# Kernel optimization log

Hardware: AMD Instinct MI355X
Metric: run time of the kernel (lower is better)

The kernel has to match this reference:

```python
import jax, jax.numpy as jnp
import numpy as np

M1 = 12; M2 = 12; WIDTH = 32; NR = 16; GROUPS = 2; EPS = 1e-5
AND_M = 5; AND_LAM = 1e-4; AND_MAXIT = 16; AND_BETA = 1.0
B = 4; H = 192; W = 192


def group_norm(x, w, b, groups=GROUPS, eps=EPS):
    bb, c, hh, ww = x.shape
    xg = x.reshape(bb, groups, c // groups, hh, ww)
    mu = xg.mean(axis=(2, 3, 4), keepdims=True)
    var = xg.var(axis=(2, 3, 4), keepdims=True)
    xn = ((xg - mu) / jnp.sqrt(var + eps)).reshape(bb, c, hh, ww)
    return xn * w[None, :, None, None] + b[None, :, None, None]


def spectral_conv(z, w1, w2):
    bb, c, hh, ww = z.shape
    zf = jnp.fft.rfft2(z, axes=(-2, -1))  # (B,C,H,W//2+1) complex64
    top = jnp.einsum('bixy,ioxy->boxy', zf[:, :, :M1, :M2], w1)
    bot = jnp.einsum('bixy,ioxy->boxy', zf[:, :, hh - M1:, :M2], w2)
    out = jnp.zeros(zf.shape, zf.dtype)
    out = out.at[:, :, :M1, :M2].set(top).at[:, :, hh - M1:, :M2].set(bot)
    return jnp.fft.irfft2(out, s=(hh, ww), axes=(-2, -1))


def f_block(z, xin, p):
    (conv_w, gnw, gnb, q_w, q_b, w1r, w1i, w2r, w2i,
     w0w, w0b, n1w, n1b, n2w, n2b) = p
    # ConvInjection: conv3x3 -> GroupNorm -> channel Linear -> sigmoid
    xi = jax.lax.conv_general_dilated(xin, conv_w, (1, 1), 'SAME',
                                      dimension_numbers=('NCHW', 'OIHW', 'NCHW'))
    xi = group_norm(xi, gnw, gnb)
    xi = jax.nn.sigmoid(jnp.einsum('bnhw,dn->bdhw', xi, q_w) + q_b[None, :, None, None])
    # FourierLayer: spectral conv + 1x1 conv, gelu
    y1 = spectral_conv(z, jax.lax.complex(w1r, w1i), jax.lax.complex(w2r, w2i))
    y2 = jnp.einsum('bchw,oc->bohw', z, w0w) + w0b[None, :, None, None]
    y = jax.nn.gelu(y1 + y2, approximate=False)
    return group_norm(jax.nn.relu(z + group_norm(xi + y, n1w, n1b)), n2w, n2b)


def anderson(f, x0, m=AND_M, lam=AND_LAM, max_iter=AND_MAXIT, beta=AND_BETA):
    """Anderson acceleration; fixed iteration count (tol early-exit omitted)."""
    shp = x0.shape
    bsz = shp[0]
    fv = lambda v: f(v.reshape(shp)).reshape(bsz, -1)
    x0v = x0.reshape(bsz, -1)
    d = x0v.shape[1]
    f0 = fv(x0v)
    f1 = fv(f0)
    X = jnp.zeros((bsz, m, d), x0.dtype).at[:, 0].set(x0v).at[:, 1].set(f0)
    Fm = jnp.zeros((bsz, m, d), x0.dtype).at[:, 0].set(f0).at[:, 1].set(f1)
    last = 1
    for k in range(2, max_iter):
        n = min(k, m)
        G = Fm[:, :n] - X[:, :n]
        Hk = jnp.zeros((bsz, n + 1, n + 1), x0.dtype)
        Hk = Hk.at[:, 0, 1:].set(1.0).at[:, 1:, 0].set(1.0)
        Hk = Hk.at[:, 1:, 1:].set(jnp.einsum('bnd,bmd->bnm', G, G)
                                  + lam * jnp.eye(n, dtype=x0.dtype)[None])
        yk = jnp.zeros((bsz, n + 1, 1), x0.dtype).at[:, 0, 0].set(1.0)
        alpha = jnp.linalg.solve(Hk, yk)[:, 1:, 0]  # (B, n)
        xnew = (beta * jnp.einsum('bn,bnd->bd', alpha, Fm[:, :n])
                + (1.0 - beta) * jnp.einsum('bn,bnd->bd', alpha, X[:, :n]))
        X = X.at[:, k % m].set(xnew)
        Fm = Fm.at[:, k % m].set(fv(xnew))
        last = k % m
    return X[:, last].reshape(shp)


def setup_inputs():
    key = jax.random.key(0)
    ks = jax.random.split(key, 16)
    scale = 1.0 / (WIDTH * WIDTH)
    u = lambda k, shp, s: jax.random.uniform(k, shp, jnp.float32, -s, s)
    return {
        'x': jax.random.normal(ks[0], (B, 1, H, W), jnp.float32),
        'fc0_w': u(ks[1], (WIDTH, 1), 1.0),
        'fc0_b': u(ks[2], (WIDTH,), 1.0),
        'conv_w': 0.01 * jax.random.normal(ks[3], (NR, WIDTH, 3, 3), jnp.float32),
        'inj_gn_w': jnp.ones((NR,), jnp.float32),
        'inj_gn_b': jnp.zeros((NR,), jnp.float32),
        'q_w': 0.01 * jax.random.normal(ks[4], (WIDTH, NR), jnp.float32),
        'q_b': u(ks[5], (WIDTH,), 0.25),
        'sw1r': scale * jax.random.uniform(ks[6], (WIDTH, WIDTH, M1, M2), jnp.float32),
        'sw1i': scale * jax.random.uniform(ks[7], (WIDTH, WIDTH, M1, M2), jnp.float32),
        'sw2r': scale * jax.random.uniform(ks[8], (WIDTH, WIDTH, M1, M2), jnp.float32),
        'sw2i': scale * jax.random.uniform(ks[9], (WIDTH, WIDTH, M1, M2), jnp.float32),
        'w0_w': u(ks[10], (WIDTH, WIDTH), 1.0 / np.sqrt(WIDTH)),
        'w0_b': u(ks[11], (WIDTH,), 1.0 / np.sqrt(WIDTH)),
        'n1_w': jnp.ones((WIDTH,), jnp.float32),
        'n1_b': jnp.zeros((WIDTH,), jnp.float32),
        'n2_w': jnp.ones((WIDTH,), jnp.float32),
        'n2_b': jnp.zeros((WIDTH,), jnp.float32),
        'bn_w': jnp.ones((WIDTH,), jnp.float32),
        'bn_b': jnp.zeros((WIDTH,), jnp.float32),
        'fc1_w': u(ks[12], (32, WIDTH), 1.0 / np.sqrt(WIDTH)),
        'fc1_b': u(ks[13], (32,), 1.0 / np.sqrt(WIDTH)),
        'fc2_w': u(ks[14], (1, 32), 1.0 / np.sqrt(32.0)),
        'fc2_b': u(ks[15], (1,), 1.0 / np.sqrt(32.0)),
    }


def reference(x, fc0_w, fc0_b, conv_w, inj_gn_w, inj_gn_b, q_w, q_b,
              sw1r, sw1i, sw2r, sw2i, w0_w, w0_b, n1_w, n1_b, n2_w, n2_b,
              bn_w, bn_b, fc1_w, fc1_b, fc2_w, fc2_b):
    xin = jnp.einsum('bchw,oc->bohw', x, fc0_w) + fc0_b[None, :, None, None]
    p = (conv_w, inj_gn_w, inj_gn_b, q_w, q_b, sw1r, sw1i, sw2r, sw2i,
         w0_w, w0_b, n1_w, n1_b, n2_w, n2_b)
    z_star = anderson(lambda z: f_block(z, xin, p), jnp.zeros_like(xin))
    z = f_block(z_star, xin, p)
    # BatchNorm2d (training-mode batch statistics, biased var)
    mu = z.mean(axis=(0, 2, 3), keepdims=True)
    var = z.var(axis=(0, 2, 3), keepdims=True)
    zb = (z - mu) / jnp.sqrt(var + EPS) * bn_w[None, :, None, None] + bn_b[None, :, None, None]
    h1 = jax.nn.gelu(jnp.einsum('bchw,oc->bohw', zb, fc1_w) + fc1_b[None, :, None, None],
                     approximate=False)
    return jnp.einsum('bchw,oc->bohw', h1, fc2_w) + fc2_b[None, :, None, None]
```

## Files before the change

### kernel.cpp

```cpp
#include <hip/hip_runtime.h>
#include <math.h>

#ifndef M_PI
#define M_PI 3.14159265358979323846
#endif

#define BBc 4
#define CCc 32
#define NRk 16
#define HHc 192
#define WWc 192
#define HWc 36864
#define DDi 1179648
#define M1c 12
#define EPSc 1e-5f

static const size_t DDs = (size_t)DDi;

#define SZ_T   ((size_t)4718592)
#define SZ_ZC  ((size_t)589824)
#define SZ_ZF  ((size_t)73728)
#define SZ_WT  ((size_t)589824)
#define SZ_TAB ((size_t)4992)

#define OFF_XC   ((size_t)0)
#define OFF_XI   (OFF_XC + SZ_T)
#define OFF_F    (OFF_XI + SZ_T)
#define OFF_G    (OFF_F + 5 * SZ_T)
#define OFF_ZC   (OFF_G + 5 * SZ_T)
#define OFF_ZF   (OFF_ZC + SZ_ZC)
#define OFF_MO   (OFF_ZF + SZ_ZF)
#define OFF_TM   (OFF_MO + SZ_ZF)
#define OFF_WT   (OFF_TM + SZ_ZC)
#define OFF_TAB  (OFF_WT + SZ_WT)
#define OFF_STAT (OFF_TAB + SZ_TAB)
#define A_XI0  OFF_G

#define NSLICE  32
#define NGSLICE 16
#define ST_EV   1024
#define ST_INJ   (16 * ST_EV)
#define ST_BN    (ST_INJ + 16)
#define ST_GRAM  (ST_BN + 64)
#define ST_ALPHA (ST_GRAM + NGSLICE * 60)
#define ST_TOTAL (ST_ALPHA + 20)

__device__ __forceinline__ float bf2f(unsigned short u) {
    return __uint_as_float(((unsigned int)u) << 16);
}
__device__ __forceinline__ unsigned short f2bf(float f) {
    unsigned int u = __float_as_uint(f);
    unsigned int r = (u + 0x7FFFu + ((u >> 16) & 1u)) >> 16;
    return (unsigned short)r;
}

__global__ void k_zero(float* p, int n) {
    int i = blockIdx.x * blockDim.x + threadIdx.x;
    if (i < n) p[i] = 0.f;
}

__global__ void k_tables(float* tab) {
    int i = blockIdx.x * blockDim.x + threadIdx.x;
    if (i < 13 * 192) {
        int k = i / 192, x = i % 192;
        double th = 2.0 * M_PI * (double)(k * x) / 192.0;
        tab[i] = (float)cos(th);
        tab[13 * 192 + i] = (float)sin(th);
    }
}

__global__ void k_wt(const float* __restrict__ w1r, const float* __restrict__ w1i,
                     const float* __restrict__ w2r, const float* __restrict__ w2i,
                     float* __restrict__ wt) {
    int idx = blockIdx.x * 256 + threadIdx.x;
    if (idx >= 24 * 12 * 1024) return;
    int o = idx & 31;
    int i = (idx >> 5) & 31;
    int ky = (idx >> 10) % 12;
    int j = idx / (12 * 1024);
    const float* wr;
    const float* wi;
    int x;
    if (j < 12) { wr = w1r; wi = w1i; x = j; }
    else        { wr = w2r; wi = w2i; x = j - 12; }
    int src = ((i * 32 + o) * 12 + x) * 12 + ky;
    size_t dst = (((size_t)ky * 24 + j) * 1024 + i * 32 + o) * 2;
    wt[dst] = wr[src];
    wt[dst + 1] = wi[src];
}

__global__ void k_ew(const float* __restrict__ cw, const float* __restrict__ fc0w,
                     const float* __restrict__ fc0b, float* __restrict__ ewb) {
    int i = threadIdx.x;
    if (i >= 144) return;
    int n = i / 9, t = i % 9;
    float ew = 0.f, eb = 0.f;
    for (int c = 0; c < 32; ++c) {
        float k = cw[(size_t)(n * CCc + c) * 9 + t];
        ew += k * fc0w[c];
        eb += k * fc0b[c];
    }
    ewb[i] = ew;
    ewb[144 + i] = eb;
}

__global__ __launch_bounds__(192) void k_conv2(const float* __restrict__ x,
                                               const float* __restrict__ ewb,
                                               float* __restrict__ xi0) {
    int b = blockIdx.x / HHc, h = blockIdx.x % HHc;
    __shared__ float sm[3 * 194];
    __shared__ float ews[144], ebs[144];
    int w = threadIdx.x;
    for (int i = threadIdx.x; i < 3 * 194; i += 192) {
        int r = i / 194, col = (i % 194) - 1;
        int hr = h + r - 1;
        float v = 0.f;
        if (hr >= 0 && hr < HHc && col >= 0 && col < WWc)
            v = x[(size_t)b * HWc + (size_t)hr * WWc + col];
        sm[i] = v;
    }
    if (threadIdx.x < 144) {
        ews[threadIdx.x] = ewb[threadIdx.x];
        ebs[threadIdx.x] = ewb[144 + threadIdx.x];
    }
    __syncthreads();
    float xv[9], mk[9];
#pragma unroll
    for (int r = 0; r < 3; ++r) {
        int hr = h + r - 1;
        bool rok = (hr >= 0 && hr < HHc);
#pragma unroll
        for (int dx = 0; dx < 3; ++dx) {
            int wx = w + dx - 1;
            bool ok = rok && (wx >= 0) && (wx < WWc);
            xv[r * 3 + dx] = sm[r * 194 + (w + dx)];
            mk[r * 3 + dx] = ok ? 1.f : 0.f;
        }
    }
#pragma unroll
    for (int n = 0; n < 16; ++n) {
        float acc = 0.f;
#pragma unroll
        for (int t = 0; t < 9; ++t)
            acc += ews[n * 9 + t] * xv[t] + mk[t] * ebs[n * 9 + t];
        xi0[((size_t)b * NRk + n) * HWc + (size_t)h * WWc + w] = acc;
    }
}

__global__ void k_binstats(const float* __restrict__ src, float* __restrict__ stats,
                           int binsize, int blocksPerBin) {
    int bin = blockIdx.x / blocksPerBin, sub = blockIdx.x % blocksPerBin;
    const float* p = src + (size_t)bin * binsize;
    float s = 0.f, q = 0.f;
    for (int i = sub * blockDim.x + threadIdx.x; i < binsize; i += blocksPerBin * blockDim.x) {
        float v = p[i];
        s += v;
        q += v * v;
    }
    for (int o = 32; o; o >>= 1) { s += __shfl_down(s, o); q += __shfl_down(q, o); }
    __shared__ float rs[4], rq[4];
    int wid = threadIdx.x >> 6, lane = threadIdx.x & 63;
    if (lane == 0) { rs[wid] = s; rq[wid] = q; }
    __syncthreads();
    if (threadIdx.x == 0) {
        int nw = blockDim.x >> 6;
        float ts = 0.f, tq = 0.f;
        for (int i = 0; i < nw; ++i) { ts += rs[i]; tq += rq[i]; }
        atomicAdd(&stats[bin * 2], ts);
        atomicAdd(&stats[bin * 2 + 1], tq);
    }
}

__global__ __launch_bounds__(192) void k_xi(const float* __restrict__ xi0,
                                            const float* __restrict__ stats,
                                            const float* __restrict__ gnw, const float* __restrict__ gnb,
                                            const float* __restrict__ qw, const float* __restrict__ qb,
                                            float* __restrict__ xi) {
    int b = blockIdx.x / HHc, h = blockIdx.x % HHc;
    int w = threadIdx.x;
    const float Ninv = 1.f / (8.f * HWc);
    float tn[16];
#pragma unroll
    for (int n = 0; n < 16; ++n) {
        int g = n >> 3;
        float su = stats[(b * 2 + g) * 2], sq = stats[(b * 2 + g) * 2 + 1];
        float mu = su * Ninv;
        float var = sq * Ninv - mu * mu;
        float inv = rsqrtf(var + EPSc);
        float v = xi0[((size_t)b * NRk + n) * HWc + (size_t)h * WWc + w];
        tn[n] = (v - mu) * inv * gnw[n] + gnb[n];
    }
#pragma unroll
    for (int d = 0; d < 32; ++d) {
        float acc = qb[d];
        const float* row = qw + d * 16;
#pragma unroll
        for (int n = 0; n < 16; ++n) acc += tn[n] * row[n];
        xi[((size_t)b * CCc + d) * HWc + (size_t)h * WWc + w] = 1.f / (1.f + expf(-acc));
    }
}


__global__ __launch_bounds__(192) void k_dftw(const float* __restrict__ z0,
                                              const float* __restrict__ tab,
                                              float* __restrict__ Zc) {
    int bc = blockIdx.x / 24;
    int hg = blockIdx.x % 24;
    int b = bc >> 5, c = bc & 31;
    const float* zp = z0 + (size_t)b * DDs + (size_t)c * HWc + (size_t)hg * 8 * WWc;
    __shared__ float rows[8 * 196];
    __shared__ float tb[24 * 196];
    const float4* zq = (const float4*)zp;
    for (int i4 = threadIdx.x; i4 < 384; i4 += 192) {
        float4 v = zq[i4];
        int r = i4 / 48, col = (i4 % 48) * 4;
        *(float4*)&rows[r * 196 + col] = v;
    }
    for (int i4 = threadIdx.x; i4 < 1152; i4 += 192) {
        int rr = i4 / 48, col = (i4 % 48) * 4;
        const float* src = (rr < 12) ? &tab[rr * 192 + col] : &tab[2496 + (rr - 12) * 192 + col];
        *(float4*)&tb[rr * 196 + col] = *(const float4*)src;
    }
    __syncthreads();
    int t = threadIdx.x;
    int r = t / 24, q = t % 24, ky = q >> 1, isim = q & 1;
    const float* tbp = tb + (isim ? (12 + ky) * 196 : ky * 196);
    const float* rowp = rows + r * 196;
    float a0 = 0.f, a1 = 0.f, a2 = 0.f, a3 = 0.f;
#pragma unroll
    for (int w2 = 0; w2 < WWc; w2 += 4) {
        a0 += rowp[w2] * tbp[w2];
        a1 += rowp[w2 + 1] * tbp[w2 + 1];
        a2 += rowp[w2 + 2] * tbp[w2 + 2];
        a3 += rowp[w2 + 3] * tbp[w2 + 3];
    }
    float acc = (a0 + a1) + (a2 + a3);
    if (isim) acc = -acc;
    int h = hg * 8 + r;
    Zc[(((size_t)ky * 128 + bc) * HHc + h) * 2 + isim] = acc;
}

__global__ __launch_bounds__(192) void k_dftwx(const float* __restrict__ F,
                                               const float* __restrict__ gram,
                                               const float* __restrict__ tab,
                                               float* __restrict__ xc,
                                               float* __restrict__ Zc,
                                               int n) {
    int bc = blockIdx.x / 24;
    int hg = blockIdx.x % 24;
    int b = bc >> 5, c = bc & 31;
    __shared__ float rows[8 * 196];
    __shared__ float tb[24 * 196];
    __shared__ float gs[15];
    __shared__ float alf[5];
    for (int i4 = threadIdx.x; i4 < 1152; i4 += 192) {
        int rr = i4 / 48, col = (i4 % 48) * 4;
        const float* src = (rr < 12) ? &tab[rr * 192 + col] : &tab[2496 + (rr - 12) * 192 + col];
        *(float4*)&tb[rr * 196 + col] = *(const float4*)src;
    }
    if (threadIdx.x < 15) {
        float v = 0.f;
        for (int s2 = 0; s2 < NGSLICE; ++s2) v += gram[s2 * 60 + b * 15 + threadIdx.x];
        gs[threadIdx.x] = v;
    }
    __syncthreads();
    if (threadIdx.x == 0) {
        float H[5][5];
#pragma unroll
        for (int i = 0; i < 5; ++i)
#pragma unroll
            for (int j = 0; j <= i; ++j) {
                float v;
                if (i < n && j < n) v = gs[i * (i + 1) / 2 + j] + ((i == j) ? 1e-4f : 0.f);
                else                v = (i == j) ? 1.f : 0.f;
                H[i][j] = v;
                H[j][i] = v;
            }
        float L[5][5], D[5], w[5], y[5];
#pragma unroll
        for (int j = 0; j < 5; ++j) {
            float d = H[j][j];
#pragma unroll
            for (int k2 = 0; k2 < j; ++k2) d -= L[j][k2] * L[j][k2] * D[k2];
            D[j] = d;
#pragma unroll
            for (int i = j + 1; i < 5; ++i) {
                float v = H[i][j];
#pragma unroll
                for (int k2 = 0; k2 < j; ++k2) v -= L[i][k2] * L[j][k2] * D[k2];
                L[i][j] = v / d;
            }
        }
#pragma unroll
        for (int i = 0; i < 5; ++i) {
            float v = (i < n) ? 1.f : 0.f;
#pragma unroll
            for (int k2 = 0; k2 < i; ++k2) v -= L[i][k2] * w[k2];
            w[i] = v;
        }
#pragma unroll
        for (int i = 4; i >= 0; --i) {
            float v = w[i] / D[i];
#pragma unroll
            for (int k2 = i + 1; k2 < 5; ++k2) v -= L[k2][i] * y[k2];
            y[i] = v;
        }
        float sum = y[0] + y[1] + y[2] + y[3] + y[4];
        float inv = 1.f / sum;
#pragma unroll
        for (int j = 0; j < 5; ++j) alf[j] = (j < n) ? y[j] * inv : 0.f;
    }
    __syncthreads();
    float a0 = alf[0], a1 = alf[1], a2 = alf[2], a3 = alf[3], a4 = alf[4];

    size_t elem = (size_t)b * DDs + (size_t)c * HWc + (size_t)hg * 8 * WWc;
    int off4 = (int)(elem >> 2);
    const int sq4 = 1179648;
    const float4* F4 = (const float4*)F;
    float4* xc4 = (float4*)xc;
    for (int i4 = threadIdx.x; i4 < 384; i4 += 192) {
        float4 f0 = F4[off4 + i4];
        float4 f1 = F4[sq4 + off4 + i4];
        float4 f2 = F4[2 * sq4 + off4 + i4];
        float4 f3 = F4[3 * sq4 + off4 + i4];
        float4 f4v = F4[4 * sq4 + off4 + i4];
        float4 v;
        v.x = a0 * f0.x + a1 * f1.x + a2 * f2.x + a3 * f3.x + a4 * f4v.x;
        v.y = a0 * f0.y + a1 * f1.y + a2 * f2.y + a3 * f3.y + a4 * f4v.y;
        v.z = a0 * f0.z + a1 * f1.z + a2 * f2.z + a3 * f3.z + a4 * f4v.z;
        v.w = a0 * f0.w + a1 * f1.w + a2 * f2.w + a3 * f3.w + a4 * f4v.w;
        xc4[off4 + i4] = v;
        int r = i4 / 48, col = (i4 % 48) * 4;
        *(float4*)&rows[r * 196 + col] = v;
    }
    __syncthreads();
    int t = threadIdx.x;
    int r = t / 24, q = t % 24, ky = q >> 1, isim = q & 1;
    const float* tbp = tb + (isim ? (12 + ky) * 196 : ky * 196);
    const float* rowp = rows + r * 196;
    float a0s = 0.f, a1s = 0.f, a2s = 0.f, a3s = 0.f;
#pragma unroll
    for (int w2 = 0; w2 < WWc; w2 += 4) {
        a0s += rowp[w2] * tbp[w2];
        a1s += rowp[w2 + 1] * tbp[w2 + 1];
        a2s += rowp[w2 + 2] * tbp[w2 + 2];
        a3s += rowp[w2 + 3] * tbp[w2 + 3];
    }
    float acc = (a0s + a1s) + (a2s + a3s);
    if (isim) acc = -acc;
    int h = hg * 8 + r;
    Zc[(((size_t)ky * 128 + bc) * HHc + h) * 2 + isim] = acc;
}

__global__ __launch_bounds__(256) void k_spec(const float* __restrict__ ZC,
                                              const float* __restrict__ wt,
                                              const float* __restrict__ tab,
                                              float* __restrict__ Tm) {
    int b  = blockIdx.x / 12;
    int ky = blockIdx.x % 12;
    __shared__ float zc[32 * 388];
    __shared__ float tc[13 * 196];
    __shared__ float tss[13 * 196];
    __shared__ float zf[24 * 64];
    __shared__ float mo[32 * 50];
    int t = threadIdx.x;
    const float4* zsrc = (const float4*)(ZC + (size_t)(ky * BBc + b) * CCc * HHc * 2);
    for (int i4 = t; i4 < 6144; i4 += 256) {
        int c = i4 / 96, r = (i4 % 96) * 4;
        *(float4*)&zc[c * 388 + r] = zsrc[i4];
    }
    for (int i4 = t; i4 < 1248; i4 += 256) {
        int half = i4 / 624;
        int k = (i4 % 624) / 48;
        int col = (i4 % 48) * 4;
        const float* src = tab + half * 2496 + k * 192 + col;
        float* dst = (half ? tss : tc) + k * 196 + col;
        *(float4*)dst = *(const float4*)src;
    }
    __syncthreads();
    for (int p = t; p < 768; p += 256) {
        int c = p / 24, j = p % 24;
        int k = (j < 12) ? j : 24 - j;
        float sgn = (j < 12) ? 1.f : -1.f;
        const float* zp = zc + c * 388;
        const float* cp = tc + k * 196;
        const float* sp = tss + k * 196;
        float re = 0.f, im = 0.f;
#pragma unroll 4
        for (int h = 0; h < 192; ++h) {
            float zr = zp[h * 2], zi = zp[h * 2 + 1];
            float cv = cp[h], sv = sgn * sp[h];
            re += zr * cv + zi * sv;
            im += zi * cv - zr * sv;
        }
        zf[j * 64 + c * 2] = re;
        zf[j * 64 + c * 2 + 1] = im;
    }
    __syncthreads();
    const float* wky = wt + (size_t)ky * 24 * 2048;
    for (int p = t; p < 768; p += 256) {
        int j = p / 32, o = p % 32;
        const float* wp = wky + (size_t)j * 2048 + o * 2;
        const float* zj = zf + j * 64;
        float re = 0.f, im = 0.f;
#pragma unroll 8
        for (int i = 0; i < 32; ++i) {
            float ar = zj[i * 2], ai = zj[i * 2 + 1];
            float wr = wp[i * 64], wi = wp[i * 64 + 1];
            re += ar * wr - ai * wi;
            im += ar * wi + ai * wr;
        }
        mo[o * 50 + j * 2] = re;
        mo[o * 50 + j * 2 + 1] = im;
    }
    __syncthreads();
    const float scale = 1.f / 192.f;
    for (int p = t; p < 6144; p += 256) {
        int o = p / 192, h = p % 192;
        const float* mp = mo + o * 50;
        float re = 0.f, im = 0.f;
#pragma unroll
        for (int j = 0; j < 24; ++j) {
            int k = (j < 12) ? j : 24 - j;
            float sgn = (j < 12) ? 1.f : -1.f;
            float mr = mp[j * 2], mi = mp[j * 2 + 1];
            float cv = tc[k * 196 + h], sv = sgn * tss[k * 196 + h];
            re += mr * cv - mi * sv;
            im += mr * sv + mi * cv;
        }
        float* dst = Tm + ((size_t)(b * 32 + o) * HHc + h) * 24 + ky * 2;
        dst[0] = re * scale;
        dst[1] = im * scale;
    }
}

__global__ __launch_bounds__(384) void k_f5(const float* __restrict__ z0,
                                            const float* __restrict__ Tm,
                                            const float* __restrict__ xi,
                                            const float* __restrict__ w0w,
                                            const float* __restrict__ w0b,
                                            const float* __restrict__ tab,
                                            float* __restrict__ sbuf,
                                            float* __restrict__ stats_e,
                                            int use_y1) {
    int h = blockIdx.x % HHc;
    int b = blockIdx.x / HHc;
    __shared__ float zl[32 * 192];
    __shared__ float w0s[32 * 36];
    __shared__ float tms[32 * 28];
    __shared__ float redc[6][2];
    int tid = threadIdx.x;
    int oq = tid & 3;
    int wq = (tid >> 2) % 48;
    int oh = tid / 192;
    int w4 = wq * 4;
    int ob = oh * 16 + oq;

    if (z0) {
        const float* zp = z0 + (size_t)b * DDs + (size_t)h * WWc;
        for (int i4 = tid; i4 < 32 * 48; i4 += 384) {
            int c = i4 / 48, q = (i4 % 48) * 4;
            float4 v = *(const float4*)(zp + (size_t)c * HWc + q);
            *(float4*)&zl[c * 192 + q] = v;
        }
        if (tid < 256) {
            int oo = tid >> 3, q = (tid & 7) * 4;
            *(float4*)&w0s[oo * 36 + q] = *(const float4*)(w0w + oo * 32 + q);
        }
    }
    if (use_y1) {
        if (tid < 192) {
            int oo = tid / 6, q = (tid % 6) * 4;
            *(float4*)&tms[oo * 28 + q] =
                *(const float4*)(Tm + (((size_t)b * 32 + oo) * HHc + h) * 24 + q);
        }
    }
    float4 c1r = *(const float4*)(tab + 192 + w4);
    float4 s1r = *(const float4*)(tab + 2496 + 192 + w4);
    __syncthreads();

    const float Winv = 1.f / 192.f;
    float acc[4][4];
#pragma unroll
    for (int oo = 0; oo < 4; ++oo) {
        float bbv = w0b[ob + oo * 4];
#pragma unroll
        for (int k = 0; k < 4; ++k) acc[oo][k] = bbv;
    }
    if (use_y1) {
#pragma unroll
        for (int oo = 0; oo < 4; ++oo) {
            float t0 = tms[(ob + oo * 4) * 28];
#pragma unroll
            for (int k = 0; k < 4; ++k) acc[oo][k] += t0 * Winv;
        }
        float4 ck = c1r, sk = s1r;
        const float sc = 2.f * Winv;
#pragma unroll
        for (int ky = 1; ky <= 11; ++ky) {
#pragma unroll
            for (int oo = 0; oo < 4; ++oo) {
                int o = ob + oo * 4;
                float tre = tms[o * 28 + 2 * ky] * sc;
                float tim = tms[o * 28 + 2 * ky + 1] * sc;
                acc[oo][0] += tre * ck.x - tim * sk.x;
                acc[oo][1] += tre * ck.y - tim * sk.y;
                acc[oo][2] += tre * ck.z - tim * sk.z;
                acc[oo][3] += tre * ck.w - tim * sk.w;
            }
            if (ky < 11) {
                float4 cn, sn;
                cn.x = ck.x * c1r.x - sk.x * s1r.x;
                sn.x = sk.x * c1r.x + ck.x * s1r.x;
                cn.y = ck.y * c1r.y - sk.y * s1r.y;
                sn.y = sk.y * c1r.y + ck.y * s1r.y;
                cn.z = ck.z * c1r.z - sk.z * s1r.z;
                sn.z = sk.z * c1r.z + ck.z * s1r.z;
                cn.w = ck.w * c1r.w - sk.w * s1r.w;
                sn.w = sk.w * c1r.w + ck.w * s1r.w;
                ck = cn; sk = sn;
            }
        }
    }
    if (z0) {
#pragma unroll 2
        for (int c = 0; c < 32; c += 4) {
            float4 wv[4];
#pragma unroll
            for (int oo = 0; oo < 4; ++oo)
                wv[oo] = *(const float4*)&w0s[(ob + oo * 4) * 36 + c];
#pragma unroll
            for (int k = 0; k < 4; ++k) {
                float4 z4 = *(const float4*)&zl[(c + k) * 192 + w4];
#pragma unroll
                for (int oo = 0; oo < 4; ++oo) {
                    float wvk = ((const float*)&wv[oo])[k];
                    acc[oo][0] += z4.x * wvk;
                    acc[oo][1] += z4.y * wvk;
                    acc[oo][2] += z4.z * wvk;
                    acc[oo][3] += z4.w * wvk;
                }
            }
        }
    }
    float4 xv[4];
#pragma unroll
    for (int oo = 0; oo < 4; ++oo) {
        int o = ob + oo * 4;
        xv[oo] = *(const float4*)(xi + (size_t)b * DDs + (size_t)o * HWc +
                                  (size_t)h * WWc + w4);
    }
    float s = 0.f, q = 0.f;
#pragma unroll
    for (int oo = 0; oo < 4; ++oo) {
        int o = ob + oo * 4;
        size_t gi = (size_t)b * DDs + (size_t)o * HWc + (size_t)h * WWc + w4;
        float4 out4;
        float* op = (float*)&out4;
        const float* xp = (const float*)&xv[oo];
#pragma unroll
        for (int k = 0; k < 4; ++k) {
            float v = acc[oo][k];
            float u = 0.5f * v * (1.f + erff(v * 0.70710678118654752f));
            float sv = xp[k] + u;
            op[k] = sv;
            s += sv;
            q += sv * sv;
        }
        *(float4*)(sbuf + gi) = out4;
    }
    for (int o2 = 32; o2; o2 >>= 1) {
        s += __shfl_down(s, o2);
        q += __shfl_down(q, o2);
    }
    int wid = tid >> 6, lane = tid & 63;
    if (lane == 0) { redc[wid][0] = s; redc[wid][1] = q; }
    __syncthreads();
    if (tid == 0) {
        float s0 = redc[0][0] + redc[1][0] + redc[2][0];
        float q0 = redc[0][1] + redc[1][1] + redc[2][1];
        float s1 = redc[3][0] + redc[4][0] + redc[5][0];
        float q1 = redc[3][1] + redc[4][1] + redc[5][1];
        int slice = blockIdx.x & (NSLICE - 1);
        float* st = stats_e + slice * 32;
        atomicAdd(&st[b * 4 + 0], s0);
        atomicAdd(&st[b * 4 + 1], q0);
        atomicAdd(&st[b * 4 + 2], s1);
        atomicAdd(&st[b * 4 + 3], q1);
    }
}

__global__ __launch_bounds__(256) void k_f6(const float* __restrict__ z0,
                                            float* buf,
                                            float* __restrict__ stats_e,
                                            const float* __restrict__ n1w,
                                            const float* __restrict__ n1b,
                                            float* __restrict__ gram,
                                            int slot) {
    {
        int gid = blockIdx.x * 256 + threadIdx.x;
        if (gid < NGSLICE * 20) {
            int s2 = gid / 20, r = gid % 20;
            int j = r % 5, b2 = r / 5;
            int ii = slot > j ? slot : j, jj = slot > j ? j : slot;
            gram[s2 * 60 + b2 * 15 + ii * (ii + 1) / 2 + jj] = 0.f;
        }
    }
    const int binq = 147456;
    const int BPB = 144;
    int bin = blockIdx.x / BPB, sub = blockIdx.x % BPB;
    float Nv = 16.f * HWc;
    float su = 0.f, sq = 0.f;
    for (int s2 = 0; s2 < NSLICE; ++s2) {
        su += stats_e[s2 * 32 + bin * 2];
        sq += stats_e[s2 * 32 + bin * 2 + 1];
    }
    float mu = su / Nv;
    float var = sq / Nv - mu * mu;
    float inv = rsqrtf(var + EPSc);
    const float4* z4 = (const float4*)z0;
    float4* b4 = (float4*)buf;
    float s = 0.f, q = 0.f;
    for (int i4 = sub * 256 + threadIdx.x; i4 < binq; i4 += BPB * 256) {
        int e4 = bin * binq + i4;
        int c = (bin & 1) * 16 + i4 / 9216;
        float w1 = inv * n1w[c];
        float b1 = n1b[c] - mu * w1;
        float4 sv = b4[e4];
        float4 zv = make_float4(0.f, 0.f, 0.f, 0.f);
        if (z0) zv = z4[e4];
        float4 r;
        r.x = zv.x + sv.x * w1 + b1; r.x = r.x > 0.f ? r.x : 0.f;
        r.y = zv.y + sv.y * w1 + b1; r.y = r.y > 0.f ? r.y : 0.f;
        r.z = zv.z + sv.z * w1 + b1; r.z = r.z > 0.f ? r.z : 0.f;
        r.w = zv.w + sv.w * w1 + b1; r.w = r.w > 0.f ? r.w : 0.f;
        b4[e4] = r;
        s += r.x + r.y + r.z + r.w;
        q += r.x * r.x + r.y * r.y + r.z * r.z + r.w * r.w;
    }
    for (int o = 32; o; o >>= 1) { s += __shfl_down(s, o); q += __shfl_down(q, o); }
    __shared__ float rs[4], rq[4];
    int wid = threadIdx.x >> 6, lane = threadIdx.x & 63;
    if (lane == 0) { rs[wid] = s; rq[wid] = q; }
    __syncthreads();
    if (threadIdx.x == 0) {
        int slice = blockIdx.x & (NSLICE - 1);
        atomicAdd(&stats_e[slice * 32 + 16 + bin * 2], rs[0] + rs[1] + rs[2] + rs[3]);
        atomicAdd(&stats_e[slice * 32 + 16 + bin * 2 + 1], rq[0] + rq[1] + rq[2] + rq[3]);
    }
}

__global__ __launch_bounds__(256) void k_f7g(float* buf,
                                             const float* __restrict__ z,
                                             const float* __restrict__ stats_e,
                                             const float* __restrict__ n2w,
                                             const float* __restrict__ n2b,
                                             unsigned short* __restrict__ G,
                                             float* __restrict__ gram,
                                             int slot, int do_gram) {
    int b = blockIdx.x / 288, sub = blockIdx.x % 288;
    const float Ninv = 1.f / (16.f * HWc);
    float su0 = 0.f, sq0 = 0.f, su1 = 0.f, sq1 = 0.f;
    for (int s2 = 0; s2 < NSLICE; ++s2) {
        const float* st = stats_e + s2 * 32 + 16 + b * 4;
        su0 += st[0]; sq0 += st[1]; su1 += st[2]; sq1 += st[3];
    }
    float mu0 = su0 * Ninv, inv0 = rsqrtf(sq0 * Ninv - mu0 * mu0 + EPSc);
    float mu1 = su1 * Ninv, inv1 = rsqrtf(sq1 * Ninv - mu1 * mu1 + EPSc);
    const int bq = 294912;
    const int sq4 = 1179648;
    float4* b4 = (float4*)buf;
    const float4* z4 = (const float4*)z;
    ushort4* GU = (ushort4*)G;
    float p0 = 0, p1 = 0, p2 = 0, p3 = 0, p4 = 0;
    for (int loc4 = sub * 256 + threadIdx.x; loc4 < bq; loc4 += 73728) {
        int e4 = b * bq + loc4;
        int c = loc4 / 9216;
        float mu = (c < 16) ? mu0 : mu1;
        float inv = (c < 16) ? inv0 : inv1;
        float wv = inv * n2w[c];
        float bv = n2b[c] - mu * wv;
        float4 r = b4[e4];
        float4 fn;
        fn.x = r.x * wv + bv;
        fn.y = r.y * wv + bv;
        fn.z = r.z * wv + bv;
        fn.w = r.w * wv + bv;
        b4[e4] = fn;
        if (do_gram) {
            float4 zv = make_float4(0.f, 0.f, 0.f, 0.f);
            if (z) zv = z4[e4];
            float4 g;
            g.x = fn.x - zv.x; g.y = fn.y - zv.y; g.z = fn.z - zv.z; g.w = fn.w - zv.w;
            ushort4 gw;
            gw.x = f2bf(g.x); gw.y = f2bf(g.y); gw.z = f2bf(g.z); gw.w = f2bf(g.w);
            GU[(size_t)slot * sq4 + e4] = gw;
            float4 gj[5];
#pragma unroll
            for (int j = 0; j < 5; ++j) {
                if (j == slot) { gj[j] = g; }
                else {
                    ushort4 u = GU[(size_t)j * sq4 + e4];
                    gj[j].x = bf2f(u.x); gj[j].y = bf2f(u.y);
                    gj[j].z = bf2f(u.z); gj[j].w = bf2f(u.w);
                }
            }
            p0 += g.x * gj[0].x + g.y * gj[0].y + g.z * gj[0].z + g.w * gj[0].w;
            p1 += g.x * gj[1].x + g.y * gj[1].y + g.z * gj[1].z + g.w * gj[1].w;
            p2 += g.x * gj[2].x + g.y * gj[2].y + g.z * gj[2].z + g.w * gj[2].w;
            p3 += g.x * gj[3].x + g.y * gj[3].y + g.z * gj[3].z + g.w * gj[3].w;
            p4 += g.x * gj[4].x + g.y * gj[4].y + g.z * gj[4].z + g.w * gj[4].w;
        }
    }
    if (!do_gram) return;
    float p[5] = {p0, p1, p2, p3, p4};
    __shared__ float red[4][5];
    int wid = threadIdx.x >> 6, lane = threadIdx.x & 63;
#pragma unroll
    for (int j = 0; j < 5; ++j) {
        float v = p[j];
        for (int o = 32; o; o >>= 1) v += __shfl_down(v, o);
        if (lane == 0) red[wid][j] = v;
    }
    __syncthreads();
    if (threadIdx.x == 0) {
        int gsl = (blockIdx.x & (NGSLICE - 1)) * 60;
#pragma unroll
        for (int j = 0; j < 5; ++j) {
            int ii = slot > j ? slot : j, jj = slot > j ? j : slot;
            atomicAdd(&gram[gsl + b * 15 + ii * (ii + 1) / 2 + jj],
                      red[0][j] + red[1][j] + red[2][j] + red[3][j]);
        }
    }
}

__global__ __launch_bounds__(256) void k_bnstats(const float* __restrict__ z,
                                                 float* __restrict__ bstats) {
    const int BPB = 18;
    int c = blockIdx.x / BPB, sub = blockIdx.x % BPB;
    float s = 0.f, q = 0.f;
    for (int i = sub * 256 + threadIdx.x; i < BBc * HWc; i += BPB * 256) {
        int b = i / HWc, hw = i % HWc;
        float v = z[(size_t)b * DDs + (size_t)c * HWc + hw];
        s += v;
        q += v * v;
    }
    for (int o = 32; o; o >>= 1) { s += __shfl_down(s, o); q += __shfl_down(q, o); }
    __shared__ float rs[4], rq[4];
    int wid = threadIdx.x >> 6, lane = threadIdx.x & 63;
    if (lane == 0) { rs[wid] = s; rq[wid] = q; }
    __syncthreads();
    if (threadIdx.x == 0) {
        atomicAdd(&bstats[c * 2], rs[0] + rs[1] + rs[2] + rs[3]);
        atomicAdd(&bstats[c * 2 + 1], rq[0] + rq[1] + rq[2] + rq[3]);
    }
}

__global__ __launch_bounds__(192) void k_final(const float* __restrict__ z,
                                               const float* __restrict__ bstats,
                                               const float* __restrict__ bnw,
                                               const float* __restrict__ bnb,
                                               const float* __restrict__ fc1w,
                                               const float* __restrict__ fc1b,
                                               const float* __restrict__ fc2w,
                                               const float* __restrict__ fc2b,
                                               float* __restrict__ out) {
    int b = blockIdx.x / HHc, h = blockIdx.x % HHc;
    int w = threadIdx.x;
    const float Ninv = 1.f / ((float)BBc * HWc);
    float zv[32];
#pragma unroll
    for (int c = 0; c < 32; ++c) {
        float su = bstats[c * 2], sq = bstats[c * 2 + 1];
        float mu = su * Ninv;
        float var = sq * Ninv - mu * mu;
        float inv = rsqrtf(var + EPSc);
        float v = z[(size_t)b * DDs + (size_t)c * HWc + (size_t)h * WWc + w];
        zv[c] = (v - mu) * inv * bnw[c] + bnb[c];
    }
    float acc2 = fc2b[0];
#pragma unroll
    for (int o = 0; o < 32; ++o) {
        float a = fc1b[o];
        const float* row = fc1w + o * 32;
#pragma unroll
        for (int c = 0; c < 32; ++c) a += zv[c] * row[c];
        float g = 0.5f * a * (1.f + erff(a * 0.70710678118654752f));
        acc2 += fc2w[o] * g;
    }
    out[(size_t)b * HWc + (size_t)h * WWc + w] = acc2;
}

extern "C" void kernel_launch(void* const* d_in, const int* in_sizes, int n_in,
                              void* d_out, int out_size, void* d_ws, size_t ws_size,
                              hipStream_t stream) {
    (void)in_sizes; (void)n_in; (void)out_size; (void)ws_size;
    const float* x    = (const float*)d_in[0];
    const float* fc0w = (const float*)d_in[1];
    const float* fc0b = (const float*)d_in[2];
    const float* convw = (const float*)d_in[3];
    const float* gnw  = (const float*)d_in[4];
    const float* gnb  = (const float*)d_in[5];
    const float* qw   = (const float*)d_in[6];
    const float* qb   = (const float*)d_in[7];
    const float* sw1r = (const float*)d_in[8];
    const float* sw1i = (const float*)d_in[9];
    const float* sw2r = (const float*)d_in[10];
    const float* sw2i = (const float*)d_in[11];
    const float* w0w  = (const float*)d_in[12];
    const float* w0b  = (const float*)d_in[13];
    const float* n1w  = (const float*)d_in[14];
    const float* n1b  = (const float*)d_in[15];
    const float* n2w  = (const float*)d_in[16];
    const float* n2b  = (const float*)d_in[17];
    const float* bnw  = (const float*)d_in[18];
    const float* bnb  = (const float*)d_in[19];
    const float* fc1w = (const float*)d_in[20];
    const float* fc1b = (const float*)d_in[21];
    const float* fc2w = (const float*)d_in[22];
    const float* fc2b = (const float*)d_in[23];
    float* out = (float*)d_out;

    float* ws = (float*)d_ws;
    float* XC  = ws + OFF_XC;
    float* XIp = ws + OFF_XI;
    float* Fb  = ws + OFF_F;
    unsigned short* Gb16 = (unsigned short*)(ws + OFF_G);
    float* ZC  = ws + OFF_ZC;
    float* MOp = ws + OFF_MO;
    float* TM  = ws + OFF_TM;
    float* WT  = ws + OFF_WT;
    float* TAB = ws + OFF_TAB;
    float* ST  = ws + OFF_STAT;
    float* XI0 = ws + A_XI0;
    float* EWB = MOp;

    auto runtail = [&](const float* zin, int outslot, int use_y1, int evalIdx,
                       int do_gram) {
        float* dst = Fb + (size_t)outslot * SZ_T;
        if (use_y1) {
            k_spec<<<BBc * 12, 256, 0, stream>>>(ZC, WT, TAB, TM);
        }
        float* stats_e = ST + (size_t)evalIdx * ST_EV;
        k_f5<<<BBc * HHc, 384, 0, stream>>>(zin, TM, XIp, w0w, w0b, TAB, dst,
                                            stats_e, use_y1);
        k_f6<<<8 * 144, 256, 0, stream>>>(zin, dst, stats_e, n1w, n1b,
                                          ST + ST_GRAM, outslot);
        k_f7g<<<4 * 288, 256, 0, stream>>>(dst, zin, stats_e, n2w, n2b, Gb16,
                                           ST + ST_GRAM, outslot, do_gram);
    };

    k_tables<<<10, 256, 0, stream>>>(TAB);
    k_wt<<<(24 * 12 * 1024 + 255) / 256, 256, 0, stream>>>(sw1r, sw1i, sw2r, sw2i, WT);
    k_zero<<<(ST_TOTAL + 255) / 256, 256, 0, stream>>>(ST, ST_TOTAL);
    k_ew<<<1, 192, 0, stream>>>(convw, fc0w, fc0b, EWB);
    k_conv2<<<BBc * HHc, 192, 0, stream>>>(x, EWB, XI0);
    k_binstats<<<8 * 36, 256, 0, stream>>>(XI0, ST + ST_INJ, 8 * HWc, 36);
    k_xi<<<BBc * HHc, 192, 0, stream>>>(XI0, ST + ST_INJ, gnw, gnb, qw, qb, XIp);

    runtail(nullptr, 0, 0, 0, 1);
    k_dftw<<<BBc * CCc * 24, 192, 0, stream>>>(Fb, TAB, ZC);
    runtail(Fb, 1, 1, 1, 1);

    for (int k = 2; k < 16; ++k) {
        int n = k < 5 ? k : 5;
        int slot = k % 5;
        k_dftwx<<<BBc * CCc * 24, 192, 0, stream>>>(Fb, ST + ST_GRAM, TAB, XC, ZC, n);
        runtail(XC, slot, 1, k, (k < 15) ? 1 : 0);
    }

    k_bnstats<<<32 * 18, 256, 0, stream>>>(Fb, ST + ST_BN);
    k_final<<<BBc * HHc, 192, 0, stream>>>(Fb, ST + ST_BN, bnw, bnb, fc1w, fc1b,
                                           fc2w, fc2b, out);
}
```

Measured before the change: 2.106 ms.

## Split spectral kernel into two stages to raise block parallelism

The single k_spec kernel ran only 48 blocks, each doing the H-direction DFT for all 32 channels, the channel mixing, and the inverse H-DFT. It is now split into k_specA, which runs 256 blocks each computing the forward H-DFT for one (b,c) and half the ky modes, and k_specB, which runs 192 blocks each doing the channel mixing and the inverse DFT for a quarter of the rows. The aim is to fill far more of the GPU's compute units and shrink per-block shared memory. The cost is an extra launch, an intermediate ZF buffer round trip through global memory, and the channel-mixing step now repeated in each of the four row-quarter blocks.

```diff
diff --git a/kernel.cpp b/kernel.cpp
--- a/kernel.cpp
+++ b/kernel.cpp
@@ -352,49 +352,76 @@
     Zc[(((size_t)ky * 128 + bc) * HHc + h) * 2 + isim] = acc;
 }
 
-__global__ __launch_bounds__(256) void k_spec(const float* __restrict__ ZC,
-                                              const float* __restrict__ wt,
-                                              const float* __restrict__ tab,
-                                              float* __restrict__ Tm) {
-    int b  = blockIdx.x / 12;
-    int ky = blockIdx.x % 12;
-    __shared__ float zc[32 * 388];
-    __shared__ float tc[13 * 196];
-    __shared__ float tss[13 * 196];
+
+__global__ __launch_bounds__(192) void k_specA(const float* __restrict__ ZC,
+                                               const float* __restrict__ tab,
+                                               float* __restrict__ ZF) {
+    int kyh = blockIdx.x & 1;
+    int c = (blockIdx.x >> 1) & 31;
+    int b = blockIdx.x >> 6;
+    int bc = b * 32 + c;
+    int ky0 = kyh * 6;
+    __shared__ float zc[6 * 388];
+    __shared__ float tcs[13 * 196];
+    __shared__ float tsn[13 * 196];
+    int t = threadIdx.x;
+    for (int i4 = t; i4 < 576; i4 += 192) {
+        int kyl = i4 / 96, r4 = (i4 % 96) * 4;
+        *(float4*)&zc[kyl * 388 + r4] =
+            *(const float4*)(ZC + (size_t)((ky0 + kyl) * 128 + bc) * 384 + r4);
+    }
+    for (int i4 = t; i4 < 1248; i4 += 192) {
+        int half = i4 / 624, k = (i4 % 624) / 48, col = (i4 % 48) * 4;
+        const float* src = tab + half * 2496 + k * 192 + col;
+        float* dst = (half ? tsn : tcs) + k * 196 + col;
+        *(float4*)dst = *(const float4*)src;
+    }
+    __syncthreads();
+    if (t < 144) {
+        int kyl = t / 24, j = t % 24;
+        int k = (j < 12) ? j : 24 - j;
+        float sgn = (j < 12) ? 1.f : -1.f;
+        const float* zp = zc + kyl * 388;
+        const float* cp = tcs + k * 196;
+        const float* sp = tsn + k * 196;
+        float re0 = 0.f, im0 = 0.f, re1 = 0.f, im1 = 0.f;
+        for (int h = 0; h < 192; h += 2) {
+            float zr = zp[h * 2], zi = zp[h * 2 + 1];
+            float cv = cp[h], sv = sgn * sp[h];
+            re0 += zr * cv + zi * sv;
+            im0 += zi * cv - zr * sv;
+            float zr1 = zp[h * 2 + 2], zi1 = zp[h * 2 + 3];
+            float cv1 = cp[h + 1], sv1 = sgn * sp[h + 1];
+            re1 += zr1 * cv1 + zi1 * sv1;
+            im1 += zi1 * cv1 - zr1 * sv1;
+        }
+        size_t o = (((size_t)(b * 12 + ky0 + kyl) * 24 + j) * 32 + c) * 2;
+        ZF[o] = re0 + re1;
+        ZF[o + 1] = im0 + im1;
+    }
+}
+
+__global__ __launch_bounds__(256) void k_specB(const float* __restrict__ ZF,
+                                               const float* __restrict__ wt,
+                                               const float* __restrict__ tab,
+                                               float* __restrict__ Tm) {
+    int hq = blockIdx.x & 3;
+    int ky = (blockIdx.x >> 2) % 12;
+    int b = blockIdx.x / 48;
     __shared__ float zf[24 * 64];
     __shared__ float mo[32 * 50];
+    __shared__ float tcs[13 * 48];
+    __shared__ float tsn[13 * 48];
     int t = threadIdx.x;
-    const float4* zsrc = (const float4*)(ZC + (size_t)(ky * BBc + b) * CCc * HHc * 2);
-    for (int i4 = t; i4 < 6144; i4 += 256) {
-        int c = i4 / 96, r = (i4 % 96) * 4;
-        *(float4*)&zc[c * 388 + r] = zsrc[i4];
-    }
-    for (int i4 = t; i4 < 1248; i4 += 256) {
-        int half = i4 / 624;
-        int k = (i4 % 624) / 48;
-        int col = (i4 % 48) * 4;
-        const float* src = tab + half * 2496 + k * 192 + col;
-        float* dst = (half ? tss : tc) + k * 196 + col;
+    const float4* zsrc = (const float4*)(ZF + (size_t)(b * 12 + ky) * 1536);
+    for (int i4 = t; i4 < 384; i4 += 256)
+        *(float4*)&zf[i4 * 4] = zsrc[i4];
+    for (int i4 = t; i4 < 312; i4 += 256) {
+        int half = i4 / 156, idx = i4 % 156;
+        int k = idx / 12, col = (idx % 12) * 4;
+        const float* src = tab + half * 2496 + k * 192 + hq * 48 + col;
+        float* dst = (half ? tsn : tcs) + k * 48 + col;
         *(float4*)dst = *(const float4*)src;
-    }
-    __syncthreads();
-    for (int p = t; p < 768; p += 256) {
-        int c = p / 24, j = p % 24;
-        int k = (j < 12) ? j : 24 - j;
-        float sgn = (j < 12) ? 1.f : -1.f;
-        const float* zp = zc + c * 388;
-        const float* cp = tc + k * 196;
-        const float* sp = tss + k * 196;
-        float re = 0.f, im = 0.f;
-#pragma unroll 4
-        for (int h = 0; h < 192; ++h) {
-            float zr = zp[h * 2], zi = zp[h * 2 + 1];
-            float cv = cp[h], sv = sgn * sp[h];
-            re += zr * cv + zi * sv;
-            im += zi * cv - zr * sv;
-        }
-        zf[j * 64 + c * 2] = re;
-        zf[j * 64 + c * 2 + 1] = im;
     }
     __syncthreads();
     const float* wky = wt + (size_t)ky * 24 * 2048;
@@ -415,8 +442,9 @@
     }
     __syncthreads();
     const float scale = 1.f / 192.f;
-    for (int p = t; p < 6144; p += 256) {
-        int o = p / 192, h = p % 192;
+    for (int p = t; p < 1536; p += 256) {
+        int o = p / 48, hl = p % 48;
+        int h = hq * 48 + hl;
         const float* mp = mo + o * 50;
         float re = 0.f, im = 0.f;
 #pragma unroll
@@ -424,7 +452,7 @@
             int k = (j < 12) ? j : 24 - j;
             float sgn = (j < 12) ? 1.f : -1.f;
             float mr = mp[j * 2], mi = mp[j * 2 + 1];
-            float cv = tc[k * 196 + h], sv = sgn * tss[k * 196 + h];
+            float cv = tcs[k * 48 + hl], sv = sgn * tsn[k * 48 + hl];
             re += mr * cv - mi * sv;
             im += mr * sv + mi * cv;
         }
@@ -827,6 +855,7 @@
     float* Fb  = ws + OFF_F;
     unsigned short* Gb16 = (unsigned short*)(ws + OFF_G);
     float* ZC  = ws + OFF_ZC;
+    float* ZFp = ws + OFF_ZF;
     float* MOp = ws + OFF_MO;
     float* TM  = ws + OFF_TM;
     float* WT  = ws + OFF_WT;
@@ -839,7 +868,8 @@
                        int do_gram) {
         float* dst = Fb + (size_t)outslot * SZ_T;
         if (use_y1) {
-            k_spec<<<BBc * 12, 256, 0, stream>>>(ZC, WT, TAB, TM);
+            k_specA<<<256, 192, 0, stream>>>(ZC, TAB, ZFp);
+            k_specB<<<BBc * 12 * 4, 256, 0, stream>>>(ZFp, WT, TAB, TM);
         }
         float* stats_e = ST + (size_t)evalIdx * ST_EV;
         k_f5<<<BBc * HHc, 384, 0, stream>>>(zin, TM, XIp, w0w, w0b, TAB, dst,
```

After: 1.776 ms. -15.7%, faster.
